# Kernel optimization log

Measured on AMD Instinct MI355X. Metric: run time of the kernel, lower is better.

## Reference

```python
import jax, jax.numpy as jnp
import numpy as np

EPS = 1e-5

def _ln(x, g, b):
    mu = jnp.mean(x, axis=-1, keepdims=True)
    var = jnp.var(x, axis=-1, keepdims=True)
    return (x - mu) * jax.lax.rsqrt(var + EPS) * g + b

def setup_inputs() -> dict:
    key = jax.random.key(0)
    ks = jax.random.split(key, 12)
    T, B, D, H = 64, 2048, 512, 512
    seq = jax.random.normal(ks[0], (T, B, D), dtype=jnp.float32)
    ts = jnp.sort(jax.random.uniform(ks[1], (B, T), dtype=jnp.float32) * 10.0, axis=1)
    def xavier(k, shape):
        fan_in, fan_out = shape[1], shape[0]
        lim = float(np.sqrt(6.0 / (fan_in + fan_out)))
        return jax.random.uniform(k, shape, jnp.float32, -lim, lim)
    Wr = xavier(ks[2], (H, D + H)); br = jnp.ones((H,), jnp.float32)   # reset bias init 1.0
    Wz = xavier(ks[3], (H, D + H)); bz = jnp.ones((H,), jnp.float32)   # update bias init 1.0
    Wc = xavier(ks[4], (H, D + H)); bc = jnp.zeros((H,), jnp.float32)
    Wo = xavier(ks[5], (H, H));     bo = jnp.zeros((H,), jnp.float32)  # output projection
    gx = jnp.ones((D,), jnp.float32); bx = jnp.zeros((D,), jnp.float32)  # layer_norm_x
    gh = jnp.ones((H,), jnp.float32); bh = jnp.zeros((H,), jnp.float32)  # layer_norm_h
    gc = jnp.ones((H,), jnp.float32); bcell = jnp.zeros((H,), jnp.float32)  # layer_norm_out (cell)
    gf = jnp.ones((H,), jnp.float32); bf = jnp.zeros((H,), jnp.float32)  # final layer_norm
    return {"seq": seq, "time_stamps": ts,
            "Wr": Wr, "br": br, "Wz": Wz, "bz": bz, "Wc": Wc, "bc": bc,
            "Wo": Wo, "bo": bo, "gx": gx, "bx": bx, "gh": gh, "bh": bh,
            "gc": gc, "bcell": bcell, "gf": gf, "bf": bf}

def _cell(xn, hn, Wr, br, Wz, bz, Wc, bc, gc, bcell):
    # xn: normalized input [B,D]; hn: (normalized, time-scaled) hidden [B,H]
    xh = jnp.concatenate([xn, hn], axis=-1)
    r = jax.nn.sigmoid(xh @ Wr.T + br)
    z = jax.nn.sigmoid(xh @ Wz.T + bz)
    xrh = jnp.concatenate([xn, r * hn], axis=-1)
    h_tilde = jnp.tanh(xrh @ Wc.T + bc)
    h_new = (1.0 - z) * hn + z * h_tilde
    return _ln(h_new, gc, bcell)  # cell output layer norm (dropout is identity in eval)

def reference(seq, time_stamps, Wr, br, Wz, bz, Wc, bc, Wo, bo, gx, bx, gh, bh, gc, bcell, gf, bf):
    T, B, D = seq.shape
    # first step: h is None -> zeros, no LN on h, no time-decay
    x0 = _ln(seq[0], gx, bx)
    h0 = _cell(x0, jnp.zeros((B, Wr.shape[0]), seq.dtype), Wr, br, Wz, bz, Wc, bc, gc, bcell)
    # remaining steps under scan with LN(h) and exp(-dt) decay
    dts = (time_stamps[:, 1:] - time_stamps[:, :-1]).T  # [T-1, B]
    def step(h, inp):
        x_t, dt = inp
        xn = _ln(x_t, gx, bx)
        hn = _ln(h, gh, bh) * jnp.exp(-jnp.clip(dt, 0.0, 10.0))[:, None]
        h_new = _cell(xn, hn, Wr, br, Wz, bz, Wc, bc, gc, bcell)
        return h_new, h_new
    _, rest = jax.lax.scan(step, h0, (seq[1:], dts))
    states = jnp.concatenate([h0[None], rest], axis=0)  # [T,B,H]
    out = jnp.einsum('tbh,oh->tbo', states, Wo) + bo
    out = out + seq  # residual (input_dim == hidden_dim); dropout identity in eval
    return _ln(out, gf, bf)
```

## Files before the change

### kernel.cpp

```cpp
#include <hip/hip_runtime.h>
#include <math.h>

#define TT 64
#define BB 2048

using f32x4   = __attribute__((ext_vector_type(4))) float;
using short8  = __attribute__((ext_vector_type(8))) short;
using short4v = __attribute__((ext_vector_type(4))) short;

__device__ __forceinline__ unsigned short f2bf(float f) {
    unsigned u = __float_as_uint(f);
    u += 0x7FFF + ((u >> 16) & 1);
    return (unsigned short)(u >> 16);
}
__device__ __forceinline__ float bf2f(unsigned short h) {
    return __uint_as_float(((unsigned)h) << 16);
}
__device__ __forceinline__ float sigmoidf_(float v) { return 1.0f / (1.0f + expf(-v)); }
__device__ __forceinline__ float tanhf_(float v)    { return 1.0f - 2.0f / (expf(2.0f * v) + 1.0f); }

__global__ __launch_bounds__(256)
void cvt_kernel(const float* __restrict__ src, unsigned short* __restrict__ dst, int n) {
    int i = blockIdx.x * 256 + threadIdx.x;
    if (i < n) dst[i] = f2bf(src[i]);
}

__global__ __launch_bounds__(256)
void pack_w2(const float* __restrict__ src, unsigned short* __restrict__ dst,
             int N, int Ksrc, int kbeg, int Kpk) {
    int i = blockIdx.x * 256 + threadIdx.x;
    if (i >= N * Kpk) return;
    int n = i / Kpk, k = i - n * Kpk;
    int dstIdx = ((n >> 4) * (Kpk >> 5) + (k >> 5)) * 512 + (((k >> 3) & 3) * 16 + (n & 15)) * 8 + (k & 7);
    dst[dstIdx] = f2bf(src[(size_t)n * Ksrc + kbeg + k]);
}

__device__ __forceinline__ int pk_idx(int row, int col) {
    int ks = col >> 5, khi = (col >> 3) & 3, j = col & 7;
    return ((ks * 64) + khi * 16 + row) * 8 + j;
}

__device__ __forceinline__ void ln_row_pk(const float* __restrict__ xr,
                                          const float* __restrict__ g,
                                          const float* __restrict__ b,
                                          unsigned short* __restrict__ tile,
                                          int row, int lane) {
    const int c0 = lane * 8;
    float4 v0 = *(const float4*)(xr + c0);
    float4 v1 = *(const float4*)(xr + c0 + 4);
    float s  = v0.x + v0.y + v0.z + v0.w + v1.x + v1.y + v1.z + v1.w;
    float ss = v0.x*v0.x + v0.y*v0.y + v0.z*v0.z + v0.w*v0.w
             + v1.x*v1.x + v1.y*v1.y + v1.z*v1.z + v1.w*v1.w;
#pragma unroll
    for (int m = 32; m > 0; m >>= 1) { s += __shfl_xor(s, m); ss += __shfl_xor(ss, m); }
    const float mean = s * (1.0f / 512.0f);
    const float var  = ss * (1.0f / 512.0f) - mean * mean;
    const float rs   = rsqrtf(var + 1e-5f);
    float4 g0 = *(const float4*)(g + c0);
    float4 g1 = *(const float4*)(g + c0 + 4);
    float4 b0 = *(const float4*)(b + c0);
    float4 b1 = *(const float4*)(b + c0 + 4);
    short8 o;
    o[0] = (short)f2bf((v0.x - mean) * rs * g0.x + b0.x);
    o[1] = (short)f2bf((v0.y - mean) * rs * g0.y + b0.y);
    o[2] = (short)f2bf((v0.z - mean) * rs * g0.z + b0.z);
    o[3] = (short)f2bf((v0.w - mean) * rs * g0.w + b0.w);
    o[4] = (short)f2bf((v1.x - mean) * rs * g1.x + b1.x);
    o[5] = (short)f2bf((v1.y - mean) * rs * g1.y + b1.y);
    o[6] = (short)f2bf((v1.z - mean) * rs * g1.z + b1.z);
    o[7] = (short)f2bf((v1.w - mean) * rs * g1.w + b1.w);
    *(short8*)&tile[(((lane >> 2) * 64) + (lane & 3) * 16 + row) * 8] = o;
}

__global__ __launch_bounds__(512)
void gx_kernel(const float* __restrict__ seq, const float* __restrict__ gxw,
               const float* __restrict__ bxw, const unsigned short* __restrict__ Wx3,
               unsigned short* __restrict__ gx)
{
    __shared__ unsigned short xt[4 * 8192];
    const int tid  = threadIdx.x;
    const int w    = tid >> 6;
    const int lane = tid & 63;
    const size_t m0 = (size_t)blockIdx.x * 64;
    const int t    = (int)(m0 >> 11);
    const int bloc = (int)((m0 & 2047) >> 4);

#pragma unroll
    for (int rr = 0; rr < 8; ++rr) {
        const int r = w * 8 + rr;
        ln_row_pk(seq + (m0 + r) * 512, gxw, bxw, xt + (r >> 4) * 8192, r & 15, lane);
    }
    __syncthreads();

    for (int nt = 0; nt < 3; ++nt) {
        f32x4 acc[4][4] = {};
#pragma unroll 4
        for (int ks = 0; ks < 16; ++ks) {
            short8 a[4], b[4];
#pragma unroll
            for (int mf = 0; mf < 4; ++mf)
                a[mf] = *(const short8*)&xt[mf * 8192 + (ks * 64 + lane) * 8];
#pragma unroll
            for (int nf = 0; nf < 4; ++nf)
                b[nf] = *(const short8*)(Wx3 + (size_t)(nt * 32 + w * 4 + nf) * 8192 + ks * 512 + lane * 8);
#pragma unroll
            for (int mf = 0; mf < 4; ++mf)
#pragma unroll
                for (int nf = 0; nf < 4; ++nf)
                    acc[mf][nf] = __builtin_amdgcn_mfma_f32_16x16x32_bf16(a[mf], b[nf], acc[mf][nf], 0, 0, 0);
        }
#pragma unroll
        for (int mf = 0; mf < 4; ++mf)
#pragma unroll
            for (int nf = 0; nf < 4; ++nf) {
                const size_t base = (((size_t)t * 128 + bloc + mf) * 96 + nt * 32 + w * 4 + nf) * 256 + lane * 4;
                short4v o;
                o[0] = (short)f2bf(acc[mf][nf][0]);
                o[1] = (short)f2bf(acc[mf][nf][1]);
                o[2] = (short)f2bf(acc[mf][nf][2]);
                o[3] = (short)f2bf(acc[mf][nf][3]);
                *(short4v*)&gx[base] = o;
            }
    }
}

template<int SBF, int HOIST>
__global__ __launch_bounds__(512)
void recurrent_kernel(const float* __restrict__ seq, const float* __restrict__ ts,
                      const unsigned short* __restrict__ Wrz, const unsigned short* __restrict__ Wc,
                      const float* __restrict__ br, const float* __restrict__ bz,
                      const float* __restrict__ bc,
                      const float* __restrict__ gxw, const float* __restrict__ bxw,
                      const float* __restrict__ gh, const float* __restrict__ bh,
                      const float* __restrict__ gc, const float* __restrict__ bcl,
                      const unsigned short* __restrict__ gx,
                      float* __restrict__ states_f32, unsigned short* __restrict__ states_bf)
{
    __shared__ unsigned short hn_s[16 * 512];
    __shared__ unsigned short rh_s[16 * 512];
    __shared__ unsigned short xn_s[HOIST ? 64 : 16 * 512];
    __shared__ float red_s[16][8];
    __shared__ float red_q[16][8];

    const int tid  = threadIdx.x;
    const int w    = tid >> 6;
    const int lane = tid & 63;
    const int lhi  = lane >> 4;
    const int llo  = lane & 15;
    const int m0   = blockIdx.x * 16;

    for (int i = tid; i < 1024; i += 512) *(short8*)&hn_s[i * 8] = short8{};
    if (!HOIST) {
#pragma unroll
        for (int rr = 0; rr < 2; ++rr) {
            const int r = w * 2 + rr;
            ln_row_pk(seq + (size_t)(m0 + r) * 512, gxw, bxw, xn_s, r, lane);
        }
    }
    __syncthreads();

    float zreg[4][4];

    for (int t = 0; t < TT; ++t) {
        const unsigned short* gxt = HOIST ? gx + (((size_t)t * 128 + blockIdx.x) * 96) * 256 + lane * 4 : nullptr;

        {
            f32x4 aR[4] = {}, aZ[4] = {};
            if (HOIST) {
#pragma unroll
                for (int f = 0; f < 4; ++f) {
                    short4v g1 = *(const short4v*)(gxt + (size_t)(w * 4 + f) * 256);
                    short4v g2 = *(const short4v*)(gxt + (size_t)(32 + w * 4 + f) * 256);
#pragma unroll
                    for (int i = 0; i < 4; ++i) {
                        aR[f][i] = bf2f((unsigned short)g1[i]);
                        aZ[f][i] = bf2f((unsigned short)g2[i]);
                    }
                }
#pragma unroll 4
                for (int ks = 0; ks < 16; ++ks) {
                    short8 a = *(const short8*)&hn_s[(ks * 64 + lane) * 8];
                    const int off = ks * 512 + lane * 8;
#pragma unroll
                    for (int f = 0; f < 4; ++f) {
                        short8 b1 = *(const short8*)(Wrz + (size_t)(w * 4 + f) * 8192 + off);
                        aR[f] = __builtin_amdgcn_mfma_f32_16x16x32_bf16(a, b1, aR[f], 0, 0, 0);
                        short8 b2 = *(const short8*)(Wrz + (size_t)(32 + w * 4 + f) * 8192 + off);
                        aZ[f] = __builtin_amdgcn_mfma_f32_16x16x32_bf16(a, b2, aZ[f], 0, 0, 0);
                    }
                }
            } else {
                const unsigned short* wrb = Wrz + (size_t)(w * 4) * 16384;
                const unsigned short* wzb = Wrz + (size_t)(32 + w * 4) * 16384;
#pragma unroll 4
                for (int ks = 0; ks < 16; ++ks) {
                    short8 a = *(const short8*)&xn_s[(ks * 64 + lane) * 8];
                    const int off = ks * 512 + lane * 8;
#pragma unroll
                    for (int f = 0; f < 4; ++f) {
                        short8 b1 = *(const short8*)(wrb + (size_t)f * 16384 + off);
                        aR[f] = __builtin_amdgcn_mfma_f32_16x16x32_bf16(a, b1, aR[f], 0, 0, 0);
                        short8 b2 = *(const short8*)(wzb + (size_t)f * 16384 + off);
                        aZ[f] = __builtin_amdgcn_mfma_f32_16x16x32_bf16(a, b2, aZ[f], 0, 0, 0);
                    }
                }
#pragma unroll 4
                for (int ks = 16; ks < 32; ++ks) {
                    short8 a = *(const short8*)&hn_s[((ks - 16) * 64 + lane) * 8];
                    const int off = ks * 512 + lane * 8;
#pragma unroll
                    for (int f = 0; f < 4; ++f) {
                        short8 b1 = *(const short8*)(wrb + (size_t)f * 16384 + off);
                        aR[f] = __builtin_amdgcn_mfma_f32_16x16x32_bf16(a, b1, aR[f], 0, 0, 0);
                        short8 b2 = *(const short8*)(wzb + (size_t)f * 16384 + off);
                        aZ[f] = __builtin_amdgcn_mfma_f32_16x16x32_bf16(a, b2, aZ[f], 0, 0, 0);
                    }
                }
            }
#pragma unroll
            for (int f = 0; f < 4; ++f)
#pragma unroll
                for (int i = 0; i < 4; ++i) {
                    const int row = lhi * 4 + i;
                    const int col = w * 64 + f * 16 + llo;
                    const float rr = sigmoidf_(aR[f][i] + br[col]);
                    const float hv = bf2f(hn_s[pk_idx(row, col)]);
                    rh_s[pk_idx(row, col)] = f2bf(rr * hv);
                    zreg[f][i] = sigmoidf_(aZ[f][i] + bz[col]);
                }
        }
        __syncthreads();

        f32x4 aC[4] = {};
        {
            if (HOIST) {
#pragma unroll
                for (int f = 0; f < 4; ++f) {
                    short4v g3 = *(const short4v*)(gxt + (size_t)(64 + w * 4 + f) * 256);
#pragma unroll
                    for (int i = 0; i < 4; ++i) aC[f][i] = bf2f((unsigned short)g3[i]);
                }
#pragma unroll 4
                for (int ks = 0; ks < 16; ++ks) {
                    short8 a = *(const short8*)&rh_s[(ks * 64 + lane) * 8];
                    const int off = ks * 512 + lane * 8;
#pragma unroll
                    for (int f = 0; f < 4; ++f) {
                        short8 b1 = *(const short8*)(Wc + (size_t)(w * 4 + f) * 8192 + off);
                        aC[f] = __builtin_amdgcn_mfma_f32_16x16x32_bf16(a, b1, aC[f], 0, 0, 0);
                    }
                }
            } else {
                const unsigned short* wcb = Wc + (size_t)(w * 4) * 16384;
#pragma unroll 4
                for (int ks = 0; ks < 16; ++ks) {
                    short8 a = *(const short8*)&xn_s[(ks * 64 + lane) * 8];
                    const int off = ks * 512 + lane * 8;
#pragma unroll
                    for (int f = 0; f < 4; ++f) {
                        short8 b1 = *(const short8*)(wcb + (size_t)f * 16384 + off);
                        aC[f] = __builtin_amdgcn_mfma_f32_16x16x32_bf16(a, b1, aC[f], 0, 0, 0);
                    }
                }
#pragma unroll 4
                for (int ks = 16; ks < 32; ++ks) {
                    short8 a = *(const short8*)&rh_s[((ks - 16) * 64 + lane) * 8];
                    const int off = ks * 512 + lane * 8;
#pragma unroll
                    for (int f = 0; f < 4; ++f) {
                        short8 b1 = *(const short8*)(wcb + (size_t)f * 16384 + off);
                        aC[f] = __builtin_amdgcn_mfma_f32_16x16x32_bf16(a, b1, aC[f], 0, 0, 0);
                    }
                }
            }
        }
        __syncthreads();

        {
            float hnew[4][4];
#pragma unroll
            for (int f = 0; f < 4; ++f)
#pragma unroll
                for (int i = 0; i < 4; ++i) {
                    const int row = lhi * 4 + i;
                    const int col = w * 64 + f * 16 + llo;
                    const float htil = tanhf_(aC[f][i] + bc[col]);
                    const float hv = bf2f(hn_s[pk_idx(row, col)]);
                    const float z = zreg[f][i];
                    hnew[f][i] = (1.0f - z) * hv + z * htil;
                }
#pragma unroll
            for (int i = 0; i < 4; ++i) {
                float s = hnew[0][i] + hnew[1][i] + hnew[2][i] + hnew[3][i];
                float q = hnew[0][i]*hnew[0][i] + hnew[1][i]*hnew[1][i]
                        + hnew[2][i]*hnew[2][i] + hnew[3][i]*hnew[3][i];
#pragma unroll
                for (int m = 8; m >= 1; m >>= 1) { s += __shfl_xor(s, m); q += __shfl_xor(q, m); }
                if (llo == 0) { red_s[lhi * 4 + i][w] = s; red_q[lhi * 4 + i][w] = q; }
            }
            __syncthreads();
            float mu[4], rsd[4];
#pragma unroll
            for (int i = 0; i < 4; ++i) {
                float s = 0.f, q = 0.f;
#pragma unroll
                for (int w2 = 0; w2 < 8; ++w2) { s += red_s[lhi * 4 + i][w2]; q += red_q[lhi * 4 + i][w2]; }
                const float m_ = s * (1.0f / 512.0f);
                mu[i]  = m_;
                rsd[i] = rsqrtf(q * (1.0f / 512.0f) - m_ * m_ + 1e-5f);
            }
#pragma unroll
            for (int f = 0; f < 4; ++f)
#pragma unroll
                for (int i = 0; i < 4; ++i) {
                    const int row = lhi * 4 + i;
                    const int col = w * 64 + f * 16 + llo;
                    const float h = (hnew[f][i] - mu[i]) * rsd[i] * gc[col] + bcl[col];
                    const size_t off = (size_t)t * BB * 512 + (size_t)(m0 + row) * 512 + col;
                    if (SBF) states_bf[off] = f2bf(h);
                    else     states_f32[off] = h;
                    hnew[f][i] = h;
                }
            if (t + 1 < TT) {
                __syncthreads();
#pragma unroll
                for (int i = 0; i < 4; ++i) {
                    float s = hnew[0][i] + hnew[1][i] + hnew[2][i] + hnew[3][i];
                    float q = hnew[0][i]*hnew[0][i] + hnew[1][i]*hnew[1][i]
                            + hnew[2][i]*hnew[2][i] + hnew[3][i]*hnew[3][i];
#pragma unroll
                    for (int m = 8; m >= 1; m >>= 1) { s += __shfl_xor(s, m); q += __shfl_xor(q, m); }
                    if (llo == 0) { red_s[lhi * 4 + i][w] = s; red_q[lhi * 4 + i][w] = q; }
                }
                __syncthreads();
                float dec_[4];
#pragma unroll
                for (int i = 0; i < 4; ++i) {
                    float s = 0.f, q = 0.f;
#pragma unroll
                    for (int w2 = 0; w2 < 8; ++w2) { s += red_s[lhi * 4 + i][w2]; q += red_q[lhi * 4 + i][w2]; }
                    const float m_ = s * (1.0f / 512.0f);
                    mu[i]  = m_;
                    rsd[i] = rsqrtf(q * (1.0f / 512.0f) - m_ * m_ + 1e-5f);
                    const int row = m0 + lhi * 4 + i;
                    float dtv = ts[(size_t)row * TT + t + 1] - ts[(size_t)row * TT + t];
                    dtv = fminf(fmaxf(dtv, 0.0f), 10.0f);
                    dec_[i] = expf(-dtv);
                }
#pragma unroll
                for (int f = 0; f < 4; ++f)
#pragma unroll
                    for (int i = 0; i < 4; ++i) {
                        const int row = lhi * 4 + i;
                        const int col = w * 64 + f * 16 + llo;
                        const float hv = ((hnew[f][i] - mu[i]) * rsd[i] * gh[col] + bh[col]) * dec_[i];
                        hn_s[pk_idx(row, col)] = f2bf(hv);
                    }
                if (!HOIST) {
#pragma unroll
                    for (int rr = 0; rr < 2; ++rr) {
                        const int r = w * 2 + rr;
                        ln_row_pk(seq + ((size_t)(t + 1) * BB + m0 + r) * 512, gxw, bxw, xn_s, r, lane);
                    }
                }
            }
        }
        __syncthreads();
    }
}

template<int BF>
__global__ __launch_bounds__(512)
void proj_kernel(const float* __restrict__ S, const unsigned short* __restrict__ Sb,
                 const unsigned short* __restrict__ Wo, const float* __restrict__ bo,
                 const float* __restrict__ seq, const float* __restrict__ gf,
                 const float* __restrict__ bff, float* __restrict__ out)
{
    const int tid  = threadIdx.x;
    const int wave = tid >> 6;
    const int lane = tid & 63;
    const int lhi  = lane >> 4;
    const int llo  = lane & 15;
    const long m0  = (long)blockIdx.x * 64;

    f32x4 acc[4][4] = {};
    for (int k0 = 0; k0 < 512; k0 += 32) {
        const int kk = k0 + lhi * 8;
        short8 a[4], b[4];
#pragma unroll
        for (int mf = 0; mf < 4; ++mf) {
            if (BF) {
                a[mf] = *(const short8*)(Sb + (size_t)(m0 + mf * 16 + llo) * 512 + kk);
            } else {
                const float* ap = S + (size_t)(m0 + mf * 16 + llo) * 512 + kk;
                float4 f0 = *(const float4*)ap;
                float4 f1 = *(const float4*)(ap + 4);
                short8 av;
                av[0] = (short)f2bf(f0.x); av[1] = (short)f2bf(f0.y);
                av[2] = (short)f2bf(f0.z); av[3] = (short)f2bf(f0.w);
                av[4] = (short)f2bf(f1.x); av[5] = (short)f2bf(f1.y);
                av[6] = (short)f2bf(f1.z); av[7] = (short)f2bf(f1.w);
                a[mf] = av;
            }
        }
#pragma unroll
        for (int nf = 0; nf < 4; ++nf)
            b[nf] = *(const short8*)(Wo + (size_t)(wave * 64 + nf * 16 + llo) * 512 + kk);
#pragma unroll
        for (int mf = 0; mf < 4; ++mf)
#pragma unroll
            for (int nf = 0; nf < 4; ++nf)
                acc[mf][nf] = __builtin_amdgcn_mfma_f32_16x16x32_bf16(a[mf], b[nf], acc[mf][nf], 0, 0, 0);
    }

    __shared__ float red_s[64][8];
    __shared__ float red_q[64][8];

#pragma unroll
    for (int mf = 0; mf < 4; ++mf)
#pragma unroll
        for (int i = 0; i < 4; ++i) {
            const long row = m0 + mf * 16 + lhi * 4 + i;
#pragma unroll
            for (int nf = 0; nf < 4; ++nf) {
                const int col = wave * 64 + nf * 16 + llo;
                acc[mf][nf][i] += bo[col] + seq[(size_t)row * 512 + col];
            }
        }
    float mu[4][4], rstd[4][4];
#pragma unroll
    for (int mf = 0; mf < 4; ++mf)
#pragma unroll
        for (int i = 0; i < 4; ++i) {
            float s = 0.f, q = 0.f;
#pragma unroll
            for (int nf = 0; nf < 4; ++nf) { const float v = acc[mf][nf][i]; s += v; q += v * v; }
#pragma unroll
            for (int m = 8; m >= 1; m >>= 1) { s += __shfl_xor(s, m); q += __shfl_xor(q, m); }
            if (llo == 0) { red_s[mf * 16 + lhi * 4 + i][wave] = s; red_q[mf * 16 + lhi * 4 + i][wave] = q; }
        }
    __syncthreads();
#pragma unroll
    for (int mf = 0; mf < 4; ++mf)
#pragma unroll
        for (int i = 0; i < 4; ++i) {
            const int rl = mf * 16 + lhi * 4 + i;
            float s = 0.f, q = 0.f;
#pragma unroll
            for (int w2 = 0; w2 < 8; ++w2) { s += red_s[rl][w2]; q += red_q[rl][w2]; }
            const float m_ = s * (1.0f / 512.0f);
            const float var = q * (1.0f / 512.0f) - m_ * m_;
            mu[mf][i] = m_;
            rstd[mf][i] = rsqrtf(var + 1e-5f);
        }
#pragma unroll
    for (int mf = 0; mf < 4; ++mf)
#pragma unroll
        for (int i = 0; i < 4; ++i) {
            const long row = m0 + mf * 16 + lhi * 4 + i;
#pragma unroll
            for (int nf = 0; nf < 4; ++nf) {
                const int col = wave * 64 + nf * 16 + llo;
                out[(size_t)row * 512 + col] = (acc[mf][nf][i] - mu[mf][i]) * rstd[mf][i] * gf[col] + bff[col];
            }
        }
}

extern "C" void kernel_launch(void* const* d_in, const int* in_sizes, int n_in,
                              void* d_out, int out_size, void* d_ws, size_t ws_size,
                              hipStream_t stream) {
    const float* seq = (const float*)d_in[0];
    const float* ts  = (const float*)d_in[1];
    const float* Wr  = (const float*)d_in[2];
    const float* br  = (const float*)d_in[3];
    const float* Wz  = (const float*)d_in[4];
    const float* bz  = (const float*)d_in[5];
    const float* Wc  = (const float*)d_in[6];
    const float* bc  = (const float*)d_in[7];
    const float* Wo  = (const float*)d_in[8];
    const float* bo  = (const float*)d_in[9];
    const float* gx  = (const float*)d_in[10];
    const float* bx  = (const float*)d_in[11];
    const float* gh  = (const float*)d_in[12];
    const float* bh  = (const float*)d_in[13];
    const float* gc  = (const float*)d_in[14];
    const float* bcl = (const float*)d_in[15];
    const float* gf  = (const float*)d_in[16];
    const float* bf  = (const float*)d_in[17];
    float* out = (float*)d_out;

    char* w0 = (char*)d_ws;
    char* w = w0;
    unsigned short* Wrz_full = (unsigned short*)w; w += (size_t)1024 * 1024 * 2;
    unsigned short* Wc_full  = (unsigned short*)w; w += (size_t)512 * 1024 * 2;
    unsigned short* Wrz_h    = (unsigned short*)w; w += (size_t)1024 * 512 * 2;
    unsigned short* Wc_h     = (unsigned short*)w; w += (size_t)512 * 512 * 2;
    unsigned short* Wx3      = (unsigned short*)w; w += (size_t)1536 * 512 * 2;
    unsigned short* Wo_b     = (unsigned short*)w; w += (size_t)512 * 512 * 2;

    const size_t GXB = (size_t)TT * 128 * 96 * 256 * 2;
    const size_t SBB = (size_t)TT * BB * 512 * 2;

    const bool hoist = ws_size >= (size_t)(w - w0) + GXB;
    unsigned short* gxbuf = (unsigned short*)w;
    if (hoist) w += GXB;
    const bool sbf = ws_size >= (size_t)(w - w0) + SBB;
    unsigned short* states_bf = (unsigned short*)w;

    if (hoist) {
        pack_w2<<<1024, 256, 0, stream>>>(Wr, Wrz_h, 512, 1024, 512, 512);
        pack_w2<<<1024, 256, 0, stream>>>(Wz, Wrz_h + (size_t)512 * 512, 512, 1024, 512, 512);
        pack_w2<<<1024, 256, 0, stream>>>(Wc, Wc_h, 512, 1024, 512, 512);
        pack_w2<<<1024, 256, 0, stream>>>(Wr, Wx3, 512, 1024, 0, 512);
        pack_w2<<<1024, 256, 0, stream>>>(Wz, Wx3 + (size_t)512 * 512, 512, 1024, 0, 512);
        pack_w2<<<1024, 256, 0, stream>>>(Wc, Wx3 + (size_t)2 * 512 * 512, 512, 1024, 0, 512);
    } else {
        pack_w2<<<2048, 256, 0, stream>>>(Wr, Wrz_full, 512, 1024, 0, 1024);
        pack_w2<<<2048, 256, 0, stream>>>(Wz, Wrz_full + (size_t)512 * 1024, 512, 1024, 0, 1024);
        pack_w2<<<2048, 256, 0, stream>>>(Wc, Wc_full, 512, 1024, 0, 1024);
    }
    cvt_kernel<<<(512 * 512 + 255) / 256, 256, 0, stream>>>(Wo, Wo_b, 512 * 512);

    if (hoist)
        gx_kernel<<<2048, 512, 0, stream>>>(seq, gx, bx, Wx3, gxbuf);

    const unsigned short* Wa = hoist ? Wrz_h : Wrz_full;
    const unsigned short* Wb = hoist ? Wc_h  : Wc_full;
    if (hoist) {
        if (sbf) recurrent_kernel<1,1><<<128, 512, 0, stream>>>(seq, ts, Wa, Wb, br, bz, bc, gx, bx, gh, bh, gc, bcl, gxbuf, out, states_bf);
        else     recurrent_kernel<0,1><<<128, 512, 0, stream>>>(seq, ts, Wa, Wb, br, bz, bc, gx, bx, gh, bh, gc, bcl, gxbuf, out, states_bf);
    } else {
        if (sbf) recurrent_kernel<1,0><<<128, 512, 0, stream>>>(seq, ts, Wa, Wb, br, bz, bc, gx, bx, gh, bh, gc, bcl, gxbuf, out, states_bf);
        else     recurrent_kernel<0,0><<<128, 512, 0, stream>>>(seq, ts, Wa, Wb, br, bz, bc, gx, bx, gh, bh, gc, bcl, gxbuf, out, states_bf);
    }

    if (sbf)
        proj_kernel<1><<<2048, 512, 0, stream>>>(out, states_bf, Wo_b, bo, seq, gf, bf, out);
    else
        proj_kernel<0><<<2048, 512, 0, stream>>>(out, nullptr, Wo_b, bo, seq, gf, bf, out);
}
```

Measured before the change: 1.877 ms.

## Double recurrent block to 1024 threads, keep hidden state in registers, pack states layout

The recurrent kernel now runs 16 waves per block instead of 8, so each wave owns 32 hidden columns rather than 64. This gives more MFMA parallelism per step of the latency-bound recurrence. The normalized hidden state is also kept in registers instead of being re-read from LDS, and one barrier per step is removed by using separate reduction buffers. Intermediate states and Wo are stored in the MFMA-packed layout, so the projection kernel can load contiguous fragments. The cost is more cross-wave reduction work and more registers pressured under the 1024-thread launch bound.

```diff
diff --git a/kernel.cpp b/kernel.cpp
--- a/kernel.cpp
+++ b/kernel.cpp
@@ -18,12 +18,6 @@
 }
 __device__ __forceinline__ float sigmoidf_(float v) { return 1.0f / (1.0f + expf(-v)); }
 __device__ __forceinline__ float tanhf_(float v)    { return 1.0f - 2.0f / (expf(2.0f * v) + 1.0f); }
-
-__global__ __launch_bounds__(256)
-void cvt_kernel(const float* __restrict__ src, unsigned short* __restrict__ dst, int n) {
-    int i = blockIdx.x * 256 + threadIdx.x;
-    if (i < n) dst[i] = f2bf(src[i]);
-}
 
 __global__ __launch_bounds__(256)
 void pack_w2(const float* __restrict__ src, unsigned short* __restrict__ dst,
@@ -125,7 +119,7 @@
 }
 
 template<int SBF, int HOIST>
-__global__ __launch_bounds__(512)
+__global__ __launch_bounds__(1024)
 void recurrent_kernel(const float* __restrict__ seq, const float* __restrict__ ts,
                       const unsigned short* __restrict__ Wrz, const unsigned short* __restrict__ Wc,
                       const float* __restrict__ br, const float* __restrict__ bz,
@@ -134,13 +128,13 @@
                       const float* __restrict__ gh, const float* __restrict__ bh,
                       const float* __restrict__ gc, const float* __restrict__ bcl,
                       const unsigned short* __restrict__ gx,
-                      float* __restrict__ states_f32, unsigned short* __restrict__ states_bf)
+                      float* __restrict__ states_f32, unsigned short* __restrict__ states_pk)
 {
     __shared__ unsigned short hn_s[16 * 512];
     __shared__ unsigned short rh_s[16 * 512];
-    __shared__ unsigned short xn_s[HOIST ? 64 : 16 * 512];
-    __shared__ float red_s[16][8];
-    __shared__ float red_q[16][8];
+    __shared__ unsigned short xn_s[HOIST ? 8 : 16 * 512];
+    __shared__ float red1_s[16][16], red1_q[16][16];
+    __shared__ float red2_s[16][16], red2_q[16][16];
 
     const int tid  = threadIdx.x;
     const int w    = tid >> 6;
@@ -149,221 +143,176 @@
     const int llo  = lane & 15;
     const int m0   = blockIdx.x * 16;
 
-    for (int i = tid; i < 1024; i += 512) *(short8*)&hn_s[i * 8] = short8{};
-    if (!HOIST) {
-#pragma unroll
-        for (int rr = 0; rr < 2; ++rr) {
-            const int r = w * 2 + rr;
-            ln_row_pk(seq + (size_t)(m0 + r) * 512, gxw, bxw, xn_s, r, lane);
-        }
-    }
+    *(short8*)&hn_s[tid * 8] = short8{};
+    if (!HOIST)
+        ln_row_pk(seq + (size_t)(m0 + w) * 512, gxw, bxw, xn_s, w, lane);
     __syncthreads();
 
-    float zreg[4][4];
+    float hnreg[2][4] = {};
+    float zreg[2][4];
 
     for (int t = 0; t < TT; ++t) {
         const unsigned short* gxt = HOIST ? gx + (((size_t)t * 128 + blockIdx.x) * 96) * 256 + lane * 4 : nullptr;
 
-        {
-            f32x4 aR[4] = {}, aZ[4] = {};
-            if (HOIST) {
-#pragma unroll
-                for (int f = 0; f < 4; ++f) {
-                    short4v g1 = *(const short4v*)(gxt + (size_t)(w * 4 + f) * 256);
-                    short4v g2 = *(const short4v*)(gxt + (size_t)(32 + w * 4 + f) * 256);
-#pragma unroll
-                    for (int i = 0; i < 4; ++i) {
-                        aR[f][i] = bf2f((unsigned short)g1[i]);
-                        aZ[f][i] = bf2f((unsigned short)g2[i]);
-                    }
-                }
+        f32x4 aR[2] = {}, aZ[2] = {};
+        if (HOIST) {
+#pragma unroll
+            for (int f = 0; f < 2; ++f) {
+                short4v g1 = *(const short4v*)(gxt + (size_t)(w * 2 + f) * 256);
+                short4v g2 = *(const short4v*)(gxt + (size_t)(32 + w * 2 + f) * 256);
+#pragma unroll
+                for (int i = 0; i < 4; ++i) {
+                    aR[f][i] = bf2f((unsigned short)g1[i]);
+                    aZ[f][i] = bf2f((unsigned short)g2[i]);
+                }
+            }
+#pragma unroll 2
+            for (int ks = 0; ks < 16; ++ks) {
+                short8 a = *(const short8*)&hn_s[(ks * 64 + lane) * 8];
+                const int off = ks * 512 + lane * 8;
+#pragma unroll
+                for (int f = 0; f < 2; ++f) {
+                    short8 b1 = *(const short8*)(Wrz + (size_t)(w * 2 + f) * 8192 + off);
+                    aR[f] = __builtin_amdgcn_mfma_f32_16x16x32_bf16(a, b1, aR[f], 0, 0, 0);
+                    short8 b2 = *(const short8*)(Wrz + (size_t)(32 + w * 2 + f) * 8192 + off);
+                    aZ[f] = __builtin_amdgcn_mfma_f32_16x16x32_bf16(a, b2, aZ[f], 0, 0, 0);
+                }
+            }
+        } else {
+#pragma unroll 2
+            for (int ks = 0; ks < 32; ++ks) {
+                short8 a = (ks < 16) ? *(const short8*)&xn_s[(ks * 64 + lane) * 8]
+                                     : *(const short8*)&hn_s[((ks - 16) * 64 + lane) * 8];
+                const int off = ks * 512 + lane * 8;
+#pragma unroll
+                for (int f = 0; f < 2; ++f) {
+                    short8 b1 = *(const short8*)(Wrz + (size_t)(w * 2 + f) * 16384 + off);
+                    aR[f] = __builtin_amdgcn_mfma_f32_16x16x32_bf16(a, b1, aR[f], 0, 0, 0);
+                    short8 b2 = *(const short8*)(Wrz + (size_t)(32 + w * 2 + f) * 16384 + off);
+                    aZ[f] = __builtin_amdgcn_mfma_f32_16x16x32_bf16(a, b2, aZ[f], 0, 0, 0);
+                }
+            }
+        }
+#pragma unroll
+        for (int f = 0; f < 2; ++f)
+#pragma unroll
+            for (int i = 0; i < 4; ++i) {
+                const int row = lhi * 4 + i;
+                const int col = w * 32 + f * 16 + llo;
+                const float rr = sigmoidf_(aR[f][i] + br[col]);
+                rh_s[pk_idx(row, col)] = f2bf(rr * hnreg[f][i]);
+                zreg[f][i] = sigmoidf_(aZ[f][i] + bz[col]);
+            }
+        __syncthreads();
+
+        f32x4 aC[2] = {};
+        if (HOIST) {
+#pragma unroll
+            for (int f = 0; f < 2; ++f) {
+                short4v g3 = *(const short4v*)(gxt + (size_t)(64 + w * 2 + f) * 256);
+#pragma unroll
+                for (int i = 0; i < 4; ++i) aC[f][i] = bf2f((unsigned short)g3[i]);
+            }
 #pragma unroll 4
-                for (int ks = 0; ks < 16; ++ks) {
-                    short8 a = *(const short8*)&hn_s[(ks * 64 + lane) * 8];
-                    const int off = ks * 512 + lane * 8;
-#pragma unroll
-                    for (int f = 0; f < 4; ++f) {
-                        short8 b1 = *(const short8*)(Wrz + (size_t)(w * 4 + f) * 8192 + off);
-                        aR[f] = __builtin_amdgcn_mfma_f32_16x16x32_bf16(a, b1, aR[f], 0, 0, 0);
-                        short8 b2 = *(const short8*)(Wrz + (size_t)(32 + w * 4 + f) * 8192 + off);
-                        aZ[f] = __builtin_amdgcn_mfma_f32_16x16x32_bf16(a, b2, aZ[f], 0, 0, 0);
-                    }
-                }
-            } else {
-                const unsigned short* wrb = Wrz + (size_t)(w * 4) * 16384;
-                const unsigned short* wzb = Wrz + (size_t)(32 + w * 4) * 16384;
-#pragma unroll 4
-                for (int ks = 0; ks < 16; ++ks) {
-                    short8 a = *(const short8*)&xn_s[(ks * 64 + lane) * 8];
-                    const int off = ks * 512 + lane * 8;
-#pragma unroll
-                    for (int f = 0; f < 4; ++f) {
-                        short8 b1 = *(const short8*)(wrb + (size_t)f * 16384 + off);
-                        aR[f] = __builtin_amdgcn_mfma_f32_16x16x32_bf16(a, b1, aR[f], 0, 0, 0);
-                        short8 b2 = *(const short8*)(wzb + (size_t)f * 16384 + off);
-                        aZ[f] = __builtin_amdgcn_mfma_f32_16x16x32_bf16(a, b2, aZ[f], 0, 0, 0);
-                    }
-                }
-#pragma unroll 4
-                for (int ks = 16; ks < 32; ++ks) {
-                    short8 a = *(const short8*)&hn_s[((ks - 16) * 64 + lane) * 8];
-                    const int off = ks * 512 + lane * 8;
-#pragma unroll
-                    for (int f = 0; f < 4; ++f) {
-                        short8 b1 = *(const short8*)(wrb + (size_t)f * 16384 + off);
-                        aR[f] = __builtin_amdgcn_mfma_f32_16x16x32_bf16(a, b1, aR[f], 0, 0, 0);
-                        short8 b2 = *(const short8*)(wzb + (size_t)f * 16384 + off);
-                        aZ[f] = __builtin_amdgcn_mfma_f32_16x16x32_bf16(a, b2, aZ[f], 0, 0, 0);
-                    }
-                }
-            }
-#pragma unroll
-            for (int f = 0; f < 4; ++f)
-#pragma unroll
-                for (int i = 0; i < 4; ++i) {
-                    const int row = lhi * 4 + i;
-                    const int col = w * 64 + f * 16 + llo;
-                    const float rr = sigmoidf_(aR[f][i] + br[col]);
-                    const float hv = bf2f(hn_s[pk_idx(row, col)]);
-                    rh_s[pk_idx(row, col)] = f2bf(rr * hv);
-                    zreg[f][i] = sigmoidf_(aZ[f][i] + bz[col]);
-                }
+            for (int ks = 0; ks < 16; ++ks) {
+                short8 a = *(const short8*)&rh_s[(ks * 64 + lane) * 8];
+                const int off = ks * 512 + lane * 8;
+#pragma unroll
+                for (int f = 0; f < 2; ++f) {
+                    short8 b1 = *(const short8*)(Wc + (size_t)(w * 2 + f) * 8192 + off);
+                    aC[f] = __builtin_amdgcn_mfma_f32_16x16x32_bf16(a, b1, aC[f], 0, 0, 0);
+                }
+            }
+        } else {
+#pragma unroll 2
+            for (int ks = 0; ks < 32; ++ks) {
+                short8 a = (ks < 16) ? *(const short8*)&xn_s[(ks * 64 + lane) * 8]
+                                     : *(const short8*)&rh_s[((ks - 16) * 64 + lane) * 8];
+                const int off = ks * 512 + lane * 8;
+#pragma unroll
+                for (int f = 0; f < 2; ++f) {
+                    short8 b1 = *(const short8*)(Wc + (size_t)(w * 2 + f) * 16384 + off);
+                    aC[f] = __builtin_amdgcn_mfma_f32_16x16x32_bf16(a, b1, aC[f], 0, 0, 0);
+                }
+            }
+        }
+
+        float hnew[2][4];
+#pragma unroll
+        for (int f = 0; f < 2; ++f)
+#pragma unroll
+            for (int i = 0; i < 4; ++i) {
+                const int col = w * 32 + f * 16 + llo;
+                const float htil = tanhf_(aC[f][i] + bc[col]);
+                const float z = zreg[f][i];
+                hnew[f][i] = (1.0f - z) * hnreg[f][i] + z * htil;
+            }
+#pragma unroll
+        for (int i = 0; i < 4; ++i) {
+            float s = hnew[0][i] + hnew[1][i];
+            float q = hnew[0][i]*hnew[0][i] + hnew[1][i]*hnew[1][i];
+#pragma unroll
+            for (int m = 8; m >= 1; m >>= 1) { s += __shfl_xor(s, m); q += __shfl_xor(q, m); }
+            if (llo == 0) { red1_s[lhi * 4 + i][w] = s; red1_q[lhi * 4 + i][w] = q; }
         }
         __syncthreads();
-
-        f32x4 aC[4] = {};
-        {
-            if (HOIST) {
-#pragma unroll
-                for (int f = 0; f < 4; ++f) {
-                    short4v g3 = *(const short4v*)(gxt + (size_t)(64 + w * 4 + f) * 256);
-#pragma unroll
-                    for (int i = 0; i < 4; ++i) aC[f][i] = bf2f((unsigned short)g3[i]);
-                }
-#pragma unroll 4
-                for (int ks = 0; ks < 16; ++ks) {
-                    short8 a = *(const short8*)&rh_s[(ks * 64 + lane) * 8];
-                    const int off = ks * 512 + lane * 8;
-#pragma unroll
-                    for (int f = 0; f < 4; ++f) {
-                        short8 b1 = *(const short8*)(Wc + (size_t)(w * 4 + f) * 8192 + off);
-                        aC[f] = __builtin_amdgcn_mfma_f32_16x16x32_bf16(a, b1, aC[f], 0, 0, 0);
-                    }
-                }
-            } else {
-                const unsigned short* wcb = Wc + (size_t)(w * 4) * 16384;
-#pragma unroll 4
-                for (int ks = 0; ks < 16; ++ks) {
-                    short8 a = *(const short8*)&xn_s[(ks * 64 + lane) * 8];
-                    const int off = ks * 512 + lane * 8;
-#pragma unroll
-                    for (int f = 0; f < 4; ++f) {
-                        short8 b1 = *(const short8*)(wcb + (size_t)f * 16384 + off);
-                        aC[f] = __builtin_amdgcn_mfma_f32_16x16x32_bf16(a, b1, aC[f], 0, 0, 0);
-                    }
-                }
-#pragma unroll 4
-                for (int ks = 16; ks < 32; ++ks) {
-                    short8 a = *(const short8*)&rh_s[((ks - 16) * 64 + lane) * 8];
-                    const int off = ks * 512 + lane * 8;
-#pragma unroll
-                    for (int f = 0; f < 4; ++f) {
-                        short8 b1 = *(const short8*)(wcb + (size_t)f * 16384 + off);
-                        aC[f] = __builtin_amdgcn_mfma_f32_16x16x32_bf16(a, b1, aC[f], 0, 0, 0);
-                    }
-                }
-            }
-        }
-        __syncthreads();
-
-        {
-            float hnew[4][4];
-#pragma unroll
-            for (int f = 0; f < 4; ++f)
-#pragma unroll
-                for (int i = 0; i < 4; ++i) {
-                    const int row = lhi * 4 + i;
-                    const int col = w * 64 + f * 16 + llo;
-                    const float htil = tanhf_(aC[f][i] + bc[col]);
-                    const float hv = bf2f(hn_s[pk_idx(row, col)]);
-                    const float z = zreg[f][i];
-                    hnew[f][i] = (1.0f - z) * hv + z * htil;
-                }
+        float mu[4], rsd[4];
+#pragma unroll
+        for (int i = 0; i < 4; ++i) {
+            float s = 0.f, q = 0.f;
+#pragma unroll
+            for (int w2 = 0; w2 < 16; ++w2) { s += red1_s[lhi * 4 + i][w2]; q += red1_q[lhi * 4 + i][w2]; }
+            const float m_ = s * (1.0f / 512.0f);
+            mu[i]  = m_;
+            rsd[i] = rsqrtf(q * (1.0f / 512.0f) - m_ * m_ + 1e-5f);
+        }
+#pragma unroll
+        for (int f = 0; f < 2; ++f)
 #pragma unroll
             for (int i = 0; i < 4; ++i) {
-                float s = hnew[0][i] + hnew[1][i] + hnew[2][i] + hnew[3][i];
-                float q = hnew[0][i]*hnew[0][i] + hnew[1][i]*hnew[1][i]
-                        + hnew[2][i]*hnew[2][i] + hnew[3][i]*hnew[3][i];
+                const int row = lhi * 4 + i;
+                const int col = w * 32 + f * 16 + llo;
+                const float h = (hnew[f][i] - mu[i]) * rsd[i] * gc[col] + bcl[col];
+                if (SBF) states_pk[((size_t)t * 128 + blockIdx.x) * 8192 + pk_idx(row, col)] = f2bf(h);
+                else     states_f32[(size_t)t * BB * 512 + (size_t)(m0 + row) * 512 + col] = h;
+                hnew[f][i] = h;
+            }
+        if (t + 1 < TT) {
+#pragma unroll
+            for (int i = 0; i < 4; ++i) {
+                float s = hnew[0][i] + hnew[1][i];
+                float q = hnew[0][i]*hnew[0][i] + hnew[1][i]*hnew[1][i];
 #pragma unroll
                 for (int m = 8; m >= 1; m >>= 1) { s += __shfl_xor(s, m); q += __shfl_xor(q, m); }
-                if (llo == 0) { red_s[lhi * 4 + i][w] = s; red_q[lhi * 4 + i][w] = q; }
+                if (llo == 0) { red2_s[lhi * 4 + i][w] = s; red2_q[lhi * 4 + i][w] = q; }
             }
             __syncthreads();
-            float mu[4], rsd[4];
+            float dec_[4];
 #pragma unroll
             for (int i = 0; i < 4; ++i) {
                 float s = 0.f, q = 0.f;
 #pragma unroll
-                for (int w2 = 0; w2 < 8; ++w2) { s += red_s[lhi * 4 + i][w2]; q += red_q[lhi * 4 + i][w2]; }
+                for (int w2 = 0; w2 < 16; ++w2) { s += red2_s[lhi * 4 + i][w2]; q += red2_q[lhi * 4 + i][w2]; }
                 const float m_ = s * (1.0f / 512.0f);
                 mu[i]  = m_;
                 rsd[i] = rsqrtf(q * (1.0f / 512.0f) - m_ * m_ + 1e-5f);
-            }
-#pragma unroll
-            for (int f = 0; f < 4; ++f)
+                const int grow = m0 + lhi * 4 + i;
+                float dtv = ts[(size_t)grow * TT + t + 1] - ts[(size_t)grow * TT + t];
+                dtv = fminf(fmaxf(dtv, 0.0f), 10.0f);
+                dec_[i] = expf(-dtv);
+            }
+#pragma unroll
+            for (int f = 0; f < 2; ++f)
 #pragma unroll
                 for (int i = 0; i < 4; ++i) {
                     const int row = lhi * 4 + i;
-                    const int col = w * 64 + f * 16 + llo;
-                    const float h = (hnew[f][i] - mu[i]) * rsd[i] * gc[col] + bcl[col];
-                    const size_t off = (size_t)t * BB * 512 + (size_t)(m0 + row) * 512 + col;
-                    if (SBF) states_bf[off] = f2bf(h);
-                    else     states_f32[off] = h;
-                    hnew[f][i] = h;
-                }
-            if (t + 1 < TT) {
-                __syncthreads();
-#pragma unroll
-                for (int i = 0; i < 4; ++i) {
-                    float s = hnew[0][i] + hnew[1][i] + hnew[2][i] + hnew[3][i];
-                    float q = hnew[0][i]*hnew[0][i] + hnew[1][i]*hnew[1][i]
-                            + hnew[2][i]*hnew[2][i] + hnew[3][i]*hnew[3][i];
-#pragma unroll
-                    for (int m = 8; m >= 1; m >>= 1) { s += __shfl_xor(s, m); q += __shfl_xor(q, m); }
-                    if (llo == 0) { red_s[lhi * 4 + i][w] = s; red_q[lhi * 4 + i][w] = q; }
-                }
-                __syncthreads();
-                float dec_[4];
-#pragma unroll
-                for (int i = 0; i < 4; ++i) {
-                    float s = 0.f, q = 0.f;
-#pragma unroll
-                    for (int w2 = 0; w2 < 8; ++w2) { s += red_s[lhi * 4 + i][w2]; q += red_q[lhi * 4 + i][w2]; }
-                    const float m_ = s * (1.0f / 512.0f);
-                    mu[i]  = m_;
-                    rsd[i] = rsqrtf(q * (1.0f / 512.0f) - m_ * m_ + 1e-5f);
-                    const int row = m0 + lhi * 4 + i;
-                    float dtv = ts[(size_t)row * TT + t + 1] - ts[(size_t)row * TT + t];
-                    dtv = fminf(fmaxf(dtv, 0.0f), 10.0f);
-                    dec_[i] = expf(-dtv);
-                }
-#pragma unroll
-                for (int f = 0; f < 4; ++f)
-#pragma unroll
-                    for (int i = 0; i < 4; ++i) {
-                        const int row = lhi * 4 + i;
-                        const int col = w * 64 + f * 16 + llo;
-                        const float hv = ((hnew[f][i] - mu[i]) * rsd[i] * gh[col] + bh[col]) * dec_[i];
-                        hn_s[pk_idx(row, col)] = f2bf(hv);
-                    }
-                if (!HOIST) {
-#pragma unroll
-                    for (int rr = 0; rr < 2; ++rr) {
-                        const int r = w * 2 + rr;
-                        ln_row_pk(seq + ((size_t)(t + 1) * BB + m0 + r) * 512, gxw, bxw, xn_s, r, lane);
-                    }
-                }
-            }
+                    const int col = w * 32 + f * 16 + llo;
+                    const float hv = ((hnew[f][i] - mu[i]) * rsd[i] * gh[col] + bh[col]) * dec_[i];
+                    hnreg[f][i] = hv;
+                    hn_s[pk_idx(row, col)] = f2bf(hv);
+                }
+            if (!HOIST)
+                ln_row_pk(seq + ((size_t)(t + 1) * BB + m0 + w) * 512, gxw, bxw, xn_s, w, lane);
         }
         __syncthreads();
     }
@@ -371,7 +320,7 @@
 
 template<int BF>
 __global__ __launch_bounds__(512)
-void proj_kernel(const float* __restrict__ S, const unsigned short* __restrict__ Sb,
+void proj_kernel(const float* __restrict__ S, const unsigned short* __restrict__ Spk,
                  const unsigned short* __restrict__ Wo, const float* __restrict__ bo,
                  const float* __restrict__ seq, const float* __restrict__ gf,
                  const float* __restrict__ bff, float* __restrict__ out)
@@ -382,17 +331,19 @@
     const int lhi  = lane >> 4;
     const int llo  = lane & 15;
     const long m0  = (long)blockIdx.x * 64;
+    const int t    = (int)(m0 >> 11);
+    const int blk  = (int)((m0 & 2047) >> 4);
 
     f32x4 acc[4][4] = {};
-    for (int k0 = 0; k0 < 512; k0 += 32) {
-        const int kk = k0 + lhi * 8;
+#pragma unroll 2
+    for (int ks = 0; ks < 16; ++ks) {
         short8 a[4], b[4];
 #pragma unroll
         for (int mf = 0; mf < 4; ++mf) {
             if (BF) {
-                a[mf] = *(const short8*)(Sb + (size_t)(m0 + mf * 16 + llo) * 512 + kk);
+                a[mf] = *(const short8*)(Spk + ((size_t)t * 128 + blk + mf) * 8192 + (ks * 64 + lane) * 8);
             } else {
-                const float* ap = S + (size_t)(m0 + mf * 16 + llo) * 512 + kk;
+                const float* ap = S + (size_t)(m0 + mf * 16 + llo) * 512 + ks * 32 + lhi * 8;
                 float4 f0 = *(const float4*)ap;
                 float4 f1 = *(const float4*)(ap + 4);
                 short8 av;
@@ -405,7 +356,7 @@
         }
 #pragma unroll
         for (int nf = 0; nf < 4; ++nf)
-            b[nf] = *(const short8*)(Wo + (size_t)(wave * 64 + nf * 16 + llo) * 512 + kk);
+            b[nf] = *(const short8*)(Wo + (size_t)(wave * 4 + nf) * 8192 + ks * 512 + lane * 8);
 #pragma unroll
         for (int mf = 0; mf < 4; ++mf)
 #pragma unroll
@@ -449,9 +400,8 @@
 #pragma unroll
             for (int w2 = 0; w2 < 8; ++w2) { s += red_s[rl][w2]; q += red_q[rl][w2]; }
             const float m_ = s * (1.0f / 512.0f);
-            const float var = q * (1.0f / 512.0f) - m_ * m_;
             mu[mf][i] = m_;
-            rstd[mf][i] = rsqrtf(var + 1e-5f);
+            rstd[mf][i] = rsqrtf(q * (1.0f / 512.0f) - m_ * m_ + 1e-5f);
         }
 #pragma unroll
     for (int mf = 0; mf < 4; ++mf)
@@ -496,16 +446,16 @@
     unsigned short* Wrz_h    = (unsigned short*)w; w += (size_t)1024 * 512 * 2;
     unsigned short* Wc_h     = (unsigned short*)w; w += (size_t)512 * 512 * 2;
     unsigned short* Wx3      = (unsigned short*)w; w += (size_t)1536 * 512 * 2;
-    unsigned short* Wo_b     = (unsigned short*)w; w += (size_t)512 * 512 * 2;
+    unsigned short* Wo_pk    = (unsigned short*)w; w += (size_t)512 * 512 * 2;
 
     const size_t GXB = (size_t)TT * 128 * 96 * 256 * 2;
-    const size_t SBB = (size_t)TT * BB * 512 * 2;
+    const size_t SBB = (size_t)TT * 128 * 8192 * 2;
 
     const bool hoist = ws_size >= (size_t)(w - w0) + GXB;
     unsigned short* gxbuf = (unsigned short*)w;
     if (hoist) w += GXB;
     const bool sbf = ws_size >= (size_t)(w - w0) + SBB;
-    unsigned short* states_bf = (unsigned short*)w;
+    unsigned short* states_pk = (unsigned short*)w;
 
     if (hoist) {
         pack_w2<<<1024, 256, 0, stream>>>(Wr, Wrz_h, 512, 1024, 512, 512);
@@ -519,7 +469,7 @@
         pack_w2<<<2048, 256, 0, stream>>>(Wz, Wrz_full + (size_t)512 * 1024, 512, 1024, 0, 1024);
         pack_w2<<<2048, 256, 0, stream>>>(Wc, Wc_full, 512, 1024, 0, 1024);
     }
-    cvt_kernel<<<(512 * 512 + 255) / 256, 256, 0, stream>>>(Wo, Wo_b, 512 * 512);
+    pack_w2<<<1024, 256, 0, stream>>>(Wo, Wo_pk, 512, 512, 0, 512);
 
     if (hoist)
         gx_kernel<<<2048, 512, 0, stream>>>(seq, gx, bx, Wx3, gxbuf);
@@ -527,15 +477,15 @@
     const unsigned short* Wa = hoist ? Wrz_h : Wrz_full;
     const unsigned short* Wb = hoist ? Wc_h  : Wc_full;
     if (hoist) {
-        if (sbf) recurrent_kernel<1,1><<<128, 512, 0, stream>>>(seq, ts, Wa, Wb, br, bz, bc, gx, bx, gh, bh, gc, bcl, gxbuf, out, states_bf);
-        else     recurrent_kernel<0,1><<<128, 512, 0, stream>>>(seq, ts, Wa, Wb, br, bz, bc, gx, bx, gh, bh, gc, bcl, gxbuf, out, states_bf);
+        if (sbf) recurrent_kernel<1,1><<<128, 1024, 0, stream>>>(seq, ts, Wa, Wb, br, bz, bc, gx, bx, gh, bh, gc, bcl, gxbuf, out, states_pk);
+        else     recurrent_kernel<0,1><<<128, 1024, 0, stream>>>(seq, ts, Wa, Wb, br, bz, bc, gx, bx, gh, bh, gc, bcl, gxbuf, out, states_pk);
     } else {
-        if (sbf) recurrent_kernel<1,0><<<128, 512, 0, stream>>>(seq, ts, Wa, Wb, br, bz, bc, gx, bx, gh, bh, gc, bcl, gxbuf, out, states_bf);
-        else     recurrent_kernel<0,0><<<128, 512, 0, stream>>>(seq, ts, Wa, Wb, br, bz, bc, gx, bx, gh, bh, gc, bcl, gxbuf, out, states_bf);
+        if (sbf) recurrent_kernel<1,0><<<128, 1024, 0, stream>>>(seq, ts, Wa, Wb, br, bz, bc, gx, bx, gh, bh, gc, bcl, gxbuf, out, states_pk);
+        else     recurrent_kernel<0,0><<<128, 1024, 0, stream>>>(seq, ts, Wa, Wb, br, bz, bc, gx, bx, gh, bh, gc, bcl, gxbuf, out, states_pk);
     }
 
     if (sbf)
-        proj_kernel<1><<<2048, 512, 0, stream>>>(out, states_bf, Wo_b, bo, seq, gf, bf, out);
+        proj_kernel<1><<<2048, 512, 0, stream>>>(nullptr, states_pk, Wo_pk, bo, seq, gf, bf, out);
     else
-        proj_kernel<0><<<2048, 512, 0, stream>>>(out, nullptr, Wo_b, bo, seq, gf, bf, out);
-}
+        proj_kernel<0><<<2048, 512, 0, stream>>>(out, nullptr, Wo_pk, bo, seq, gf, bf, out);
+}
```

Result: slower. 2.201 ms (+17.3%).
